# Kernel optimization log

Hardware: AMD Instinct MI355X
Metric: run time of the kernel (lower is better)

Reference implementation:

```python
import jax, jax.numpy as jnp
import numpy as np

CAPSULE_WIDE = 8
CAPSULE_TALL = 4
FEAT = 784
FV = FEAT // CAPSULE_TALL  # 196
B = 32768


def _linear_params(key, out_dim, in_dim):
    kw, kb = jax.random.split(key)
    bound = 1.0 / np.sqrt(in_dim)
    W = jax.random.uniform(kw, (out_dim, in_dim), minval=-bound, maxval=bound, dtype=jnp.float32)
    b = jax.random.uniform(kb, (out_dim,), minval=-bound, maxval=bound, dtype=jnp.float32)
    return W, b


def setup_inputs() -> dict:
    key = jax.random.key(0)
    ks = jax.random.split(key, 7)
    x = jax.random.normal(ks[0], (B, FEAT), dtype=jnp.float32)
    W1, b1 = _linear_params(ks[1], FV, FV)
    W2, b2 = _linear_params(ks[2], FV, FV)
    W3, b3 = _linear_params(ks[3], FV, FV)
    Wd1, bd1 = _linear_params(ks[4], FEAT, FEAT)
    Wd2, bd2 = _linear_params(ks[5], FEAT, FEAT)
    Wo, bo = _linear_params(ks[6], 10, FEAT)
    return {"x": x, "W1": W1, "b1": b1, "W2": W2, "b2": b2, "W3": W3, "b3": b3,
            "Wd1": Wd1, "bd1": bd1, "Wd2": Wd2, "bd2": bd2, "Wo": Wo, "bo": bo}


def reference(x, W1, b1, W2, b2, W3, b3, Wd1, bd1, Wd2, bd2, Wo, bo):
    h = x  # [B, 784]
    for _ in range(CAPSULE_WIDE):
        v = h.reshape(h.shape[0], CAPSULE_TALL, FV)  # [B, T, FV]
        q = v @ W1.T + b1  # first_copy
        k = v @ W2.T + b2  # second_copy
        u = v @ W3.T + b3  # third_copy
        scores = jnp.einsum('btf,bsf->bts', q, k)  # [B, T, T], unscaled
        probs = jax.nn.softmax(scores, axis=-1)
        h = jnp.einsum('bts,bsf->btf', probs, u).reshape(h.shape[0], -1)
    dec = jax.nn.relu(h @ Wd1.T + bd1) @ Wd2.T + bd2  # output_decoder
    return jax.nn.softmax(dec @ Wo.T + bo, axis=-1)  # output_probability
```

## Files before the change

### kernel.cpp

```cpp
#include <hip/hip_runtime.h>
#include <math.h>

#define NT 256
#define NTC 512
typedef _Float16 f16;
typedef _Float16 half8 __attribute__((ext_vector_type(8)));
typedef _Float16 half4 __attribute__((ext_vector_type(4)));
typedef float floatx4 __attribute__((ext_vector_type(4)));

#define ROWSHR_ADD(v, N) \
  (v) += __int_as_float(__builtin_amdgcn_update_dpp(0, __float_as_int(v), 0x110 | (N), 0xF, 0xF, true))

#define WD1_OFF  0
#define WD2_OFF  1433600
#define WOT_OFF  2867200
#define D8_OFF   2917376
#define HBUF_OFF 2918400
#define D1_OFF   55347200
#define WPKH_OFF 55347200
#define WPKL_OFF 56185856
#define SSE      38464

__device__ inline void glds16(const void* g, void* l) {
  __builtin_amdgcn_global_load_lds((const __attribute__((address_space(1))) void*)g,
                                   (__attribute__((address_space(3))) void*)l, 16, 0, 0);
}

__global__ void k_prep_wd(const float* __restrict__ Wd, f16* __restrict__ W16) {
  int idx = blockIdx.x * NT + threadIdx.x;
  if (idx >= 896 * 800) return;
  int n = idx / 800, k = idx - n * 800;
  W16[idx] = (f16)((n < 784 && k < 784) ? Wd[n * 784 + k] : 0.f);
}

__global__ void k_prep_wo(const float* __restrict__ Wo, float* __restrict__ WoT) {
  int idx = blockIdx.x * NT + threadIdx.x;
  if (idx >= 784 * 16) return;
  int f = idx >> 4, n = idx & 15;
  WoT[idx] = (n < 10) ? Wo[n * 784 + f] : 0.f;
}

__global__ void k_mm(const float* __restrict__ A0, const float* __restrict__ B0,
                     float* __restrict__ C0, int ta, int tb, int sA, int sB, int sC) {
  const float* A = A0 + (size_t)blockIdx.y * sA;
  const float* B = B0 + (size_t)blockIdx.y * sB;
  float*       C = C0 + (size_t)blockIdx.y * sC;
  __shared__ float red[256];
  const int tid = threadIdx.x;
  const int o = blockIdx.x * 64 + (tid & 63);
  const int ks = tid >> 6;
  float s = 0.f;
  int p = 0, r = 0;
  if (o < 196 * 196) {
    p = o / 196; r = o - p * 196;
    const int c0 = ks * 49;
    #pragma unroll 7
    for (int c = c0; c < c0 + 49; ++c) {
      float a = ta ? A[c * 196 + p] : A[p * 196 + c];
      float b = tb ? B[r * 196 + c] : B[c * 196 + r];
      s += a * b;
    }
  }
  red[tid] = s;
  __syncthreads();
  if (tid < 64 && o < 196 * 196)
    C[p * 196 + r] = red[tid] + red[tid + 64] + red[tid + 128] + red[tid + 192];
}

__global__ void k_prep_gq(const float* __restrict__ W1, const float* __restrict__ W2,
                          const float* __restrict__ W3, float* __restrict__ scr) {
  if (blockIdx.x < 601) {
    __shared__ float red[256];
    const int tid = threadIdx.x;
    const int o = blockIdx.x * 64 + (tid & 63);
    const int ks = tid >> 6;
    float s = 0.f;
    int p = 0, r = 0;
    if (o < 196 * 196) {
      p = o / 196; r = o - p * 196;
      const int c0 = ks * 49;
      #pragma unroll 7
      for (int c = c0; c < c0 + 49; ++c)
        s += W1[c * 196 + p] * W2[c * 196 + r];
    }
    red[tid] = s;
    __syncthreads();
    if (tid < 64 && o < 196 * 196)
      scr[p * 196 + r] = red[tid] + red[tid + 64] + red[tid + 128] + red[tid + 192];
  } else {
    int idx = (blockIdx.x - 601) * NT + threadIdx.x;
    if (idx < 196 * 196) scr[(size_t)SSE + idx] = W3[idx];
  }
}

__global__ void k_prep_vec(const float* __restrict__ W2, const float* __restrict__ b1,
                           const float* __restrict__ b3,
                           const float* __restrict__ G, const float* __restrict__ Qbase,
                           float* __restrict__ gtab, float* __restrict__ d8out) {
  __shared__ float z[196], cj[196], d[196], tmp[196];
  const int i = blockIdx.x;
  const int tid = threadIdx.x;
  const float* W3 = Qbase;
  for (int t = tid; t < 196; t += NT) {
    float s = 0.f;
    for (int f = 0; f < 196; ++f) s += b1[f] * W2[f * 196 + t];
    z[t] = s;
    d[t] = 0.f;
    cj[t] = b3[t];
  }
  __syncthreads();
  for (int j = 0; j < i; ++j) {
    for (int t = tid; t < 196; t += NT) {
      float s = 0.f;
      for (int c = 0; c < 196; ++c) s += W3[t * 196 + c] * cj[c];
      tmp[t] = s;
      d[t] += cj[t];
    }
    __syncthreads();
    for (int t = tid; t < 196; t += NT) cj[t] = tmp[t];
    __syncthreads();
  }
  if (i == 7) {
    for (int t = tid; t < 196; t += NT) d8out[t] = d[t] + cj[t];
  }
  for (int t = tid; t < 196; t += NT) {
    float s = z[t];
    for (int k = 0; k < 196; ++k) s += G[k * 196 + t] * d[k];
    tmp[t] = s;
  }
  __syncthreads();
  for (int t = tid; t < 196; t += NT) {
    float s;
    if (i == 0) {
      s = tmp[t];
    } else {
      const float* Qi = Qbase + (size_t)(i - 1) * SSE;
      s = 0.f;
      for (int n = 0; n < 196; ++n) s += Qi[n * 196 + t] * tmp[n];
    }
    gtab[i * 196 + t] = s;
  }
}

__global__ void k_prep_pack(const float* __restrict__ scr,
                            f16* __restrict__ Wph, f16* __restrict__ Wpl) {
  int idx = blockIdx.x * NT + threadIdx.x;
  if (idx >= 9 * 208 * 224) return;
  int s = idx / (208 * 224), rem = idx - s * (208 * 224);
  int n = rem / 224, k = rem - n * 224;
  float v = 0.f;
  if (k < 196) {
    if (n < 196) {
      if (s == 8) {
        v = scr[(size_t)8 * SSE + n * 196 + k];
      } else {
        const float* M = (s == 0) ? scr : (scr + (size_t)(16 + s - 1) * SSE);
        v = M[k * 196 + n];
      }
    } else if (n == 196 && s < 8) {
      v = scr[(size_t)23 * SSE + s * 196 + k];
    }
  }
  f16 hi = (f16)v;
  Wph[idx] = hi;
  Wpl[idx] = (f16)(v - (float)hi);
}

__global__ __launch_bounds__(NTC, 4)
void k_caps(const float* __restrict__ x,
            const f16* __restrict__ Wph, const f16* __restrict__ Wpl,
            const float* __restrict__ d8g,
            f16* __restrict__ hbuf) {
  __shared__ __align__(16) char smem[72704];
  f16*   vAhi = (f16*)smem;
  f16*   vAlo = (f16*)(smem + 29696);
  float* Sful = (float*)(smem + 59392);
  float* Rl   = (float*)(smem + 69632);
  float* Cm   = (float*)(smem + 71680);

  const int tid  = threadIdx.x;
  const int w    = tid >> 6;
  const int lane = tid & 63;
  const int l15  = lane & 15;
  const int quad = lane >> 4;
  const int e0   = blockIdx.x * 16;
  const bool haveJ1 = (w + 8) < 13;

  for (int idx = tid; idx < 16 * 196; idx += NTC) {
    int elem = idx / 196, g = idx - elem * 196;
    int t = g / 49, f = (g - t * 49) * 4;
    floatx4 v4 = *(const floatx4*)&x[(size_t)(e0 + elem) * 784 + g * 4];
    half4 h4, l4;
    #pragma unroll
    for (int q = 0; q < 4; ++q) {
      f16 h = (f16)v4[q];
      h4[q] = h;
      l4[q] = (f16)(v4[q] - (float)h);
    }
    int vo = (elem * 4 + t) * 232 + f;
    *(half4*)&vAhi[vo] = h4;
    *(half4*)&vAlo[vo] = l4;
  }
  for (int p = tid; p < 64 * 36; p += NTC) {
    int row = p / 36, c = 196 + (p - (p / 36) * 36);
    vAhi[row * 232 + c] = (f16)0;
    vAlo[row * 232 + c] = (f16)0;
  }
  for (int p = tid; p < 8 * 16 * 20; p += NTC) Sful[p] = 0.f;
  __syncthreads();

  float vv0[4][4], vv1[4][4];
  {
    int c0 = w * 16 + l15;
    int c1 = 128 + w * 16 + l15;
    #pragma unroll
    for (int mt = 0; mt < 4; ++mt)
      #pragma unroll
      for (int s = 0; s < 4; ++s) {
        int ro = ((mt * 4 + quad) * 4 + s) * 232;
        vv0[mt][s] = (float)vAhi[ro + c0] + (float)vAlo[ro + c0];
        vv1[mt][s] = haveJ1 ? ((float)vAhi[ro + c1] + (float)vAlo[ro + c1]) : 0.f;
      }
  }

  #pragma unroll 2
  for (int i = 0; i < 8; ++i) {
    floatx4 acc0[4], acc1[4];
    #pragma unroll
    for (int mt = 0; mt < 4; ++mt) {
      acc0[mt] = (floatx4){0.f, 0.f, 0.f, 0.f};
      acc1[mt] = (floatx4){0.f, 0.f, 0.f, 0.f};
    }
    const int wb0 = ((i * 208 + w * 16 + l15) * 224) + quad * 8;
    const int wb1 = ((i * 208 + (w + 8) * 16 + l15) * 224) + quad * 8;
    #pragma unroll
    for (int ks = 0; ks < 7; ++ks) {
      half8 ah[4], al[4];
      #pragma unroll
      for (int mt = 0; mt < 4; ++mt) {
        int ao = (mt * 16 + l15) * 232 + ks * 32 + quad * 8;
        ah[mt] = *(const half8*)&vAhi[ao];
        al[mt] = *(const half8*)&vAlo[ao];
      }
      {
        half8 bh = *(const half8*)&Wph[wb0 + ks * 32];
        half8 bl = *(const half8*)&Wpl[wb0 + ks * 32];
        #pragma unroll
        for (int mt = 0; mt < 4; ++mt) {
          acc0[mt] = __builtin_amdgcn_mfma_f32_16x16x32_f16(ah[mt], bh, acc0[mt], 0, 0, 0);
          acc0[mt] = __builtin_amdgcn_mfma_f32_16x16x32_f16(ah[mt], bl, acc0[mt], 0, 0, 0);
          acc0[mt] = __builtin_amdgcn_mfma_f32_16x16x32_f16(al[mt], bh, acc0[mt], 0, 0, 0);
        }
      }
      if (haveJ1) {
        half8 bh = *(const half8*)&Wph[wb1 + ks * 32];
        half8 bl = *(const half8*)&Wpl[wb1 + ks * 32];
        #pragma unroll
        for (int mt = 0; mt < 4; ++mt) {
          acc1[mt] = __builtin_amdgcn_mfma_f32_16x16x32_f16(ah[mt], bh, acc1[mt], 0, 0, 0);
          acc1[mt] = __builtin_amdgcn_mfma_f32_16x16x32_f16(ah[mt], bl, acc1[mt], 0, 0, 0);
          acc1[mt] = __builtin_amdgcn_mfma_f32_16x16x32_f16(al[mt], bh, acc1[mt], 0, 0, 0);
        }
      }
    }
    #pragma unroll
    for (int mt = 0; mt < 4; ++mt) {
      float part[16];
      #pragma unroll
      for (int t = 0; t < 4; ++t)
        #pragma unroll
        for (int s = 0; s < 4; ++s)
          part[t * 4 + s] = acc0[mt][t] * vv0[mt][s] + acc1[mt][t] * vv1[mt][s];
      #pragma unroll
      for (int p = 0; p < 16; ++p) {
        ROWSHR_ADD(part[p], 8);
        ROWSHR_ADD(part[p], 4);
        ROWSHR_ADD(part[p], 2);
        ROWSHR_ADD(part[p], 1);
      }
      if (l15 == 0) {
        int elem = mt * 4 + quad;
        #pragma unroll
        for (int t = 0; t < 4; ++t)
          #pragma unroll
          for (int s = 0; s < 4; ++s)
            atomicAdd(&Sful[(i * 16 + elem) * 20 + t * 4 + s], part[t * 4 + s]);
      }
    }
    if (w == 4 && l15 == 4) {
      #pragma unroll
      for (int mt = 0; mt < 4; ++mt)
        *(floatx4*)&Rl[i * 64 + mt * 16 + quad * 4] = acc1[mt];
    }
  }
  __syncthreads();

  if (tid < 16) {
    const int e = tid;
    float C[4][4] = {{1,0,0,0},{0,1,0,0},{0,0,1,0},{0,0,0,1}};
    #pragma unroll 1
    for (int i = 0; i < 8; ++i) {
      float M[4][4];
      #pragma unroll
      for (int a = 0; a < 4; ++a) {
        floatx4 mm = *(const floatx4*)&Sful[(i * 16 + e) * 20 + a * 4];
        #pragma unroll
        for (int b = 0; b < 4; ++b) M[a][b] = mm[b];
      }
      floatx4 rv = *(const floatx4*)&Rl[i * 64 + e * 4];
      float T1[4][4], Cr[4];
      #pragma unroll
      for (int t = 0; t < 4; ++t)
        #pragma unroll
        for (int b = 0; b < 4; ++b)
          T1[t][b] = C[t][0]*M[0][b] + C[t][1]*M[1][b] + C[t][2]*M[2][b] + C[t][3]*M[3][b];
      #pragma unroll
      for (int s = 0; s < 4; ++s)
        Cr[s] = C[s][0]*rv[0] + C[s][1]*rv[1] + C[s][2]*rv[2] + C[s][3]*rv[3];
      float P[4][4];
      #pragma unroll
      for (int t = 0; t < 4; ++t) {
        float S[4];
        #pragma unroll
        for (int s = 0; s < 4; ++s)
          S[s] = T1[t][0]*C[s][0] + T1[t][1]*C[s][1] + T1[t][2]*C[s][2] + T1[t][3]*C[s][3] + Cr[s];
        float m = fmaxf(fmaxf(S[0], S[1]), fmaxf(S[2], S[3]));
        float e0_ = __expf(S[0] - m), e1 = __expf(S[1] - m);
        float e2 = __expf(S[2] - m), e3 = __expf(S[3] - m);
        float inv = 1.f / (e0_ + e1 + e2 + e3);
        P[t][0] = e0_ * inv; P[t][1] = e1 * inv; P[t][2] = e2 * inv; P[t][3] = e3 * inv;
      }
      float Cn[4][4];
      #pragma unroll
      for (int t = 0; t < 4; ++t)
        #pragma unroll
        for (int s = 0; s < 4; ++s)
          Cn[t][s] = P[t][0]*C[0][s] + P[t][1]*C[1][s] + P[t][2]*C[2][s] + P[t][3]*C[3][s];
      #pragma unroll
      for (int t = 0; t < 4; ++t)
        #pragma unroll
        for (int s = 0; s < 4; ++s) C[t][s] = Cn[t][s];
    }
    #pragma unroll
    for (int t = 0; t < 4; ++t)
      *(floatx4*)&Cm[e * 16 + t * 4] = (floatx4){C[t][0], C[t][1], C[t][2], C[t][3]};
  }
  __syncthreads();

  {
    floatx4 acu0[4], acu1[4];
    #pragma unroll
    for (int mt = 0; mt < 4; ++mt) {
      acu0[mt] = (floatx4){0.f, 0.f, 0.f, 0.f};
      acu1[mt] = (floatx4){0.f, 0.f, 0.f, 0.f};
    }
    const int wb0 = ((8 * 208 + w * 16 + l15) * 224) + quad * 8;
    const int wb1 = ((8 * 208 + (w + 8) * 16 + l15) * 224) + quad * 8;
    #pragma unroll
    for (int ks = 0; ks < 7; ++ks) {
      half8 ah[4], al[4];
      #pragma unroll
      for (int mt = 0; mt < 4; ++mt) {
        int ao = (mt * 16 + l15) * 232 + ks * 32 + quad * 8;
        ah[mt] = *(const half8*)&vAhi[ao];
        al[mt] = *(const half8*)&vAlo[ao];
      }
      {
        half8 bh = *(const half8*)&Wph[wb0 + ks * 32];
        half8 bl = *(const half8*)&Wpl[wb0 + ks * 32];
        #pragma unroll
        for (int mt = 0; mt < 4; ++mt) {
          acu0[mt] = __builtin_amdgcn_mfma_f32_16x16x32_f16(ah[mt], bh, acu0[mt], 0, 0, 0);
          acu0[mt] = __builtin_amdgcn_mfma_f32_16x16x32_f16(ah[mt], bl, acu0[mt], 0, 0, 0);
          acu0[mt] = __builtin_amdgcn_mfma_f32_16x16x32_f16(al[mt], bh, acu0[mt], 0, 0, 0);
        }
      }
      if (haveJ1) {
        half8 bh = *(const half8*)&Wph[wb1 + ks * 32];
        half8 bl = *(const half8*)&Wpl[wb1 + ks * 32];
        #pragma unroll
        for (int mt = 0; mt < 4; ++mt) {
          acu1[mt] = __builtin_amdgcn_mfma_f32_16x16x32_f16(ah[mt], bh, acu1[mt], 0, 0, 0);
          acu1[mt] = __builtin_amdgcn_mfma_f32_16x16x32_f16(ah[mt], bl, acu1[mt], 0, 0, 0);
          acu1[mt] = __builtin_amdgcn_mfma_f32_16x16x32_f16(al[mt], bh, acu1[mt], 0, 0, 0);
        }
      }
    }
    const int f0 = w * 16 + l15;
    const int f1 = 128 + w * 16 + l15;
    const bool doF1 = haveJ1 && (f1 < 196);
    float d80 = d8g[f0];
    float d81 = doF1 ? d8g[f1] : 0.f;
    #pragma unroll
    for (int mt = 0; mt < 4; ++mt) {
      int elem = mt * 4 + quad;
      floatx4 c0 = *(const floatx4*)&Cm[elem * 16 + 0];
      floatx4 c1 = *(const floatx4*)&Cm[elem * 16 + 4];
      floatx4 c2 = *(const floatx4*)&Cm[elem * 16 + 8];
      floatx4 c3 = *(const floatx4*)&Cm[elem * 16 + 12];
      {
        floatx4 u = acu0[mt];
        float h0 = c0[0]*u[0] + c0[1]*u[1] + c0[2]*u[2] + c0[3]*u[3] + d80;
        float h1 = c1[0]*u[0] + c1[1]*u[1] + c1[2]*u[2] + c1[3]*u[3] + d80;
        float h2 = c2[0]*u[0] + c2[1]*u[1] + c2[2]*u[2] + c2[3]*u[3] + d80;
        float h3 = c3[0]*u[0] + c3[1]*u[1] + c3[2]*u[2] + c3[3]*u[3] + d80;
        size_t base = (size_t)(e0 + elem) * 800;
        hbuf[base + 0 * 196 + f0] = (f16)h0;
        hbuf[base + 1 * 196 + f0] = (f16)h1;
        hbuf[base + 2 * 196 + f0] = (f16)h2;
        hbuf[base + 3 * 196 + f0] = (f16)h3;
      }
      if (doF1) {
        floatx4 u = acu1[mt];
        float h0 = c0[0]*u[0] + c0[1]*u[1] + c0[2]*u[2] + c0[3]*u[3] + d81;
        float h1 = c1[0]*u[0] + c1[1]*u[1] + c1[2]*u[2] + c1[3]*u[3] + d81;
        float h2 = c2[0]*u[0] + c2[1]*u[1] + c2[2]*u[2] + c2[3]*u[3] + d81;
        float h3 = c3[0]*u[0] + c3[1]*u[1] + c3[2]*u[2] + c3[3]*u[3] + d81;
        size_t base = (size_t)(e0 + elem) * 800;
        hbuf[base + 0 * 196 + f1] = (f16)h0;
        hbuf[base + 1 * 196 + f1] = (f16)h1;
        hbuf[base + 2 * 196 + f1] = (f16)h2;
        hbuf[base + 3 * 196 + f1] = (f16)h3;
      }
    }
  }
  for (int idx = tid; idx < 256; idx += NTC)
    hbuf[(size_t)(e0 + (idx >> 4)) * 800 + 784 + (idx & 15)] = (f16)0;
}

__global__ __launch_bounds__(NT, 2)
void k_dec(const f16* __restrict__ A, const f16* __restrict__ Bw,
           const float* __restrict__ bias, f16* __restrict__ C, int do_relu) {
  __shared__ __align__(16) f16 As[128 * 32];
  __shared__ __align__(16) f16 Bs[128 * 32];
  const int tid = threadIdx.x, w = tid >> 6, lane = tid & 63;
  const int l15 = lane & 15, quad = lane >> 4;
  const int m0 = blockIdx.x * 128, n0 = blockIdx.y * 128;
  const int wm = w & 1, wn = w >> 1;
  const int srow = lane >> 2, soff = (lane & 3) * 8;

  floatx4 acc[4][4];
  #pragma unroll
  for (int nt = 0; nt < 4; ++nt) {
    int col = n0 + wn * 64 + nt * 16 + l15;
    float bb = (col < 784) ? bias[col] : 0.f;
    #pragma unroll
    for (int mt = 0; mt < 4; ++mt) acc[mt][nt] = (floatx4){bb, bb, bb, bb};
  }

  for (int kk = 0; kk < 25; ++kk) {
    __syncthreads();
    #pragma unroll
    for (int i = 0; i < 2; ++i) {
      int r = w * 32 + i * 16;
      glds16(&A[(size_t)(m0 + r + srow) * 800 + kk * 32 + soff], &As[r * 32]);
      glds16(&Bw[(size_t)(n0 + r + srow) * 800 + kk * 32 + soff], &Bs[r * 32]);
    }
    __syncthreads();
    half8 af[4], bf[4];
    #pragma unroll
    for (int mt = 0; mt < 4; ++mt)
      af[mt] = *(const half8*)&As[(wm * 64 + mt * 16 + l15) * 32 + quad * 8];
    #pragma unroll
    for (int nt = 0; nt < 4; ++nt)
      bf[nt] = *(const half8*)&Bs[(wn * 64 + nt * 16 + l15) * 32 + quad * 8];
    #pragma unroll
    for (int mt = 0; mt < 4; ++mt)
      #pragma unroll
      for (int nt = 0; nt < 4; ++nt)
        acc[mt][nt] = __builtin_amdgcn_mfma_f32_16x16x32_f16(af[mt], bf[nt], acc[mt][nt], 0, 0, 0);
  }

  #pragma unroll
  for (int nt = 0; nt < 4; ++nt) {
    int gcol = n0 + wn * 64 + nt * 16 + l15;
    if (gcol < 800) {
      #pragma unroll
      for (int mt = 0; mt < 4; ++mt) {
        #pragma unroll
        for (int r = 0; r < 4; ++r) {
          int grow = m0 + wm * 64 + mt * 16 + quad * 4 + r;
          float v = acc[mt][nt][r];
          if (do_relu) v = fmaxf(v, 0.f);
          C[(size_t)grow * 800 + gcol] = (f16)v;
        }
      }
    }
  }
}

__global__ __launch_bounds__(NT, 4)
void k_logits(const f16* __restrict__ d2, const float* __restrict__ WoT,
              const float* __restrict__ bo, float* __restrict__ out) {
  __shared__ __align__(16) f16 ds[16 * 800];
  __shared__ float lg[160];
  const int tid = threadIdx.x;
  const size_t e0 = (size_t)blockIdx.x * 16;
  for (int i = tid; i < 16 * 98; i += NT) {
    int e = i / 98, c = (i - e * 98) * 8;
    *(half8*)&ds[e * 800 + c] = *(const half8*)&d2[(e0 + e) * 800 + c];
  }
  __syncthreads();
  {
    int e = tid >> 4, n = tid & 15;
    const f16* dp = &ds[e * 800];
    float s = 0.f;
    #pragma unroll 4
    for (int f = 0; f < 784; ++f) s += (float)dp[f] * WoT[f * 16 + n];
    if (n < 10) lg[e * 10 + n] = s + bo[n];
  }
  __syncthreads();
  if (tid < 16) {
    float l[10], m = -1e30f;
    #pragma unroll
    for (int n = 0; n < 10; ++n) { l[n] = lg[tid * 10 + n]; m = fmaxf(m, l[n]); }
    float sum = 0.f;
    #pragma unroll
    for (int n = 0; n < 10; ++n) { l[n] = __expf(l[n] - m); sum += l[n]; }
    float inv = 1.f / sum;
    #pragma unroll
    for (int n = 0; n < 10; ++n) out[(e0 + tid) * 10 + n] = l[n] * inv;
  }
}

extern "C" void kernel_launch(void* const* d_in, const int* in_sizes, int n_in,
                              void* d_out, int out_size, void* d_ws, size_t ws_size,
                              hipStream_t stream) {
  const float* x   = (const float*)d_in[0];
  const float* W1  = (const float*)d_in[1];
  const float* b1  = (const float*)d_in[2];
  const float* W2  = (const float*)d_in[3];
  const float* W3  = (const float*)d_in[5];
  const float* b3  = (const float*)d_in[6];
  const float* Wd1 = (const float*)d_in[7];
  const float* bd1 = (const float*)d_in[8];
  const float* Wd2 = (const float*)d_in[9];
  const float* bd2 = (const float*)d_in[10];
  const float* Wo  = (const float*)d_in[11];
  const float* bo  = (const float*)d_in[12];
  float* out = (float*)d_out;

  char* ws = (char*)d_ws;
  f16*   Wd1p  = (f16*)(ws + WD1_OFF);
  f16*   Wd2p  = (f16*)(ws + WD2_OFF);
  float* WoTws = (float*)(ws + WOT_OFF);
  float* d8ws  = (float*)(ws + D8_OFF);
  f16*   hbuf  = (f16*)(ws + HBUF_OFF);
  f16*   d1buf = (f16*)(ws + D1_OFF);
  f16*   Wph   = (f16*)(ws + WPKH_OFF);
  f16*   Wpl   = (f16*)(ws + WPKL_OFF);
  float* scr   = (float*)(ws + HBUF_OFF);

  const int GSK = (196 * 196 + 63) / 64;
  const int GCP = (196 * 196 + NT - 1) / NT;

  k_prep_wd<<<(896 * 800 + NT - 1) / NT, NT, 0, stream>>>(Wd1, Wd1p);
  k_prep_wd<<<(896 * 800 + NT - 1) / NT, NT, 0, stream>>>(Wd2, Wd2p);
  k_prep_wo<<<(784 * 16 + NT - 1) / NT, NT, 0, stream>>>(Wo, WoTws);

  k_prep_gq<<<GSK + GCP, NT, 0, stream>>>(W1, W2, W3, scr);
  k_mm<<<dim3(GSK, 1), NT, 0, stream>>>(W3, W3, scr + (size_t)2 * SSE, 0, 0, 0, 0, 0);
  k_mm<<<dim3(GSK, 2), NT, 0, stream>>>(scr + (size_t)2 * SSE, scr + (size_t)1 * SSE,
                                        scr + (size_t)3 * SSE, 0, 0, 0, SSE, SSE);
  k_mm<<<dim3(GSK, 4), NT, 0, stream>>>(scr + (size_t)4 * SSE, scr + (size_t)1 * SSE,
                                        scr + (size_t)5 * SSE, 0, 0, 0, SSE, SSE);
  k_mm<<<dim3(GSK, 7), NT, 0, stream>>>(scr + (size_t)1 * SSE, scr,
                                        scr + (size_t)9 * SSE, 1, 0, SSE, 0, SSE);
  k_mm<<<dim3(GSK, 7), NT, 0, stream>>>(scr + (size_t)9 * SSE, scr + (size_t)1 * SSE,
                                        scr + (size_t)16 * SSE, 0, 0, SSE, SSE, SSE);
  k_prep_vec<<<8, NT, 0, stream>>>(W2, b1, b3, scr, scr + (size_t)1 * SSE,
                                   scr + (size_t)23 * SSE, d8ws);
  k_prep_pack<<<(9 * 208 * 224 + NT - 1) / NT, NT, 0, stream>>>(scr, Wph, Wpl);

  k_caps<<<32768 / 16, NTC, 0, stream>>>(x, Wph, Wpl, d8ws, hbuf);
  k_dec<<<dim3(32768 / 128, 7), NT, 0, stream>>>(hbuf, Wd1p, bd1, d1buf, 1);
  k_dec<<<dim3(32768 / 128, 7), NT, 0, stream>>>(d1buf, Wd2p, bd2, hbuf, 0);
  k_logits<<<32768 / 16, NT, 0, stream>>>(hbuf, WoTws, bo, out);
}
```

Before: 858.4 us.

## Batch prep kernels into fewer launches and retune caps, dec, logits kernels

```diff
diff --git a/kernel.cpp b/kernel.cpp
--- a/kernel.cpp
+++ b/kernel.cpp
@@ -14,11 +14,11 @@
 #define WD1_OFF  0
 #define WD2_OFF  1433600
 #define WOT_OFF  2867200
-#define D8_OFF   2917376
-#define HBUF_OFF 2918400
-#define D1_OFF   55347200
-#define WPKH_OFF 55347200
-#define WPKL_OFF 56185856
+#define D8_OFF   2918400
+#define HBUF_OFF 2919424
+#define D1_OFF   55348224
+#define WPKH_OFF 55348224
+#define WPKL_OFF 56186880
 #define SSE      38464
 
 __device__ inline void glds16(const void* g, void* l) {
@@ -26,120 +26,145 @@
                                    (__attribute__((address_space(3))) void*)l, 16, 0, 0);
 }
 
-__global__ void k_prep_wd(const float* __restrict__ Wd, f16* __restrict__ W16) {
-  int idx = blockIdx.x * NT + threadIdx.x;
-  if (idx >= 896 * 800) return;
-  int n = idx / 800, k = idx - n * 800;
-  W16[idx] = (f16)((n < 784 && k < 784) ? Wd[n * 784 + k] : 0.f);
-}
-
-__global__ void k_prep_wo(const float* __restrict__ Wo, float* __restrict__ WoT) {
-  int idx = blockIdx.x * NT + threadIdx.x;
-  if (idx >= 784 * 16) return;
-  int f = idx >> 4, n = idx & 15;
-  WoT[idx] = (n < 10) ? Wo[n * 784 + f] : 0.f;
-}
-
-__global__ void k_mm(const float* __restrict__ A0, const float* __restrict__ B0,
-                     float* __restrict__ C0, int ta, int tb, int sA, int sB, int sC) {
-  const float* A = A0 + (size_t)blockIdx.y * sA;
-  const float* B = B0 + (size_t)blockIdx.y * sB;
-  float*       C = C0 + (size_t)blockIdx.y * sC;
+__global__ void k_prep_io(const float* __restrict__ Wd1, const float* __restrict__ Wd2,
+                          const float* __restrict__ Wo,
+                          f16* __restrict__ W1p, f16* __restrict__ W2p,
+                          float* __restrict__ WoT) {
+  int b = blockIdx.x;
+  if (b < 5600) {
+    const float* Wd = (b < 2800) ? Wd1 : Wd2;
+    f16* W16 = (b < 2800) ? W1p : W2p;
+    int idx = (b % 2800) * NT + threadIdx.x;
+    if (idx < 896 * 800) {
+      int n = idx / 800, k = idx - n * 800;
+      W16[idx] = (f16)((n < 784 && k < 784) ? Wd[n * 784 + k] : 0.f);
+    }
+  } else {
+    int idx = (b - 5600) * NT + threadIdx.x;
+    if (idx < 16 * 800) {
+      int n = idx / 800, f = idx - n * 800;
+      WoT[idx] = (n < 10 && f < 784) ? Wo[n * 784 + f] : 0.f;
+    }
+  }
+}
+
+__global__ void k_prep_gq(const float* __restrict__ W1, const float* __restrict__ W2,
+                          const float* __restrict__ W3, float* __restrict__ scr) {
   __shared__ float red[256];
   const int tid = threadIdx.x;
-  const int o = blockIdx.x * 64 + (tid & 63);
-  const int ks = tid >> 6;
+  int b = blockIdx.x;
+  if (b < 1202) {
+    int ta = (b < 601);
+    const float* A = ta ? W1 : W3;
+    const float* B = ta ? W2 : W3;
+    float* C = ta ? scr : (scr + (size_t)2 * SSE);
+    int u = ta ? b : (b - 601);
+    int o = u * 64 + (tid & 63);
+    int ks = tid >> 6;
+    float s = 0.f;
+    int p = 0, r = 0;
+    if (o < 38416) {
+      p = o / 196; r = o - p * 196;
+      const int c0 = ks * 49;
+      #pragma unroll 7
+      for (int c = c0; c < c0 + 49; ++c) {
+        float a = ta ? A[c * 196 + p] : A[p * 196 + c];
+        s += a * B[c * 196 + r];
+      }
+    }
+    red[tid] = s;
+    __syncthreads();
+    if (tid < 64 && o < 38416)
+      C[p * 196 + r] = red[tid] + red[tid + 64] + red[tid + 128] + red[tid + 192];
+  } else {
+    int idx = (b - 1202) * NT + tid;
+    if (idx < 38416) scr[(size_t)SSE + idx] = W3[idx];
+  }
+}
+
+__constant__ int MMA[4][8] = {{2,2,1,2,0,0,0,0},{4,4,4,4,3,4,9,10},
+                              {5,6,7,11,12,0,0,0},{13,14,15,0,0,0,0,0}};
+__constant__ int MMB[4][8] = {{1,2,0,0,0,0,0,0},{1,2,3,4,0,0,1,2},
+                              {0,0,0,3,4,0,0,0},{5,6,7,0,0,0,0,0}};
+__constant__ int MMC[4][8] = {{3,4,9,10,0,0,0,0},{5,6,7,8,11,12,16,17},
+                              {13,14,15,18,19,0,0,0},{20,21,22,0,0,0,0,0}};
+__constant__ int MMT[4][8] = {{0,0,1,1,0,0,0,0},{0,0,0,0,1,1,0,0},
+                              {1,1,1,0,0,0,0,0},{0,0,0,0,0,0,0,0}};
+
+__global__ __launch_bounds__(NT, 4)
+void k_mmb(float* __restrict__ scr, int stage,
+           const float* __restrict__ W2, const float* __restrict__ b1,
+           const float* __restrict__ b3, float* __restrict__ d8out) {
+  __shared__ float red[256];
+  __shared__ float z[196], cj[196], dd[196], tmp[196];
+  const int tid = threadIdx.x;
+  const int y = blockIdx.y;
+
+  if (stage == 2 && y == 5) {
+    if (blockIdx.x >= 8) return;
+    const int i = blockIdx.x;
+    const float* G = scr;
+    const float* Qbase = scr + (size_t)SSE;
+    float* gtab = scr + (size_t)23 * SSE;
+    const float* W3c = Qbase;
+    for (int t = tid; t < 196; t += NT) {
+      float s = 0.f;
+      for (int f = 0; f < 196; ++f) s += b1[f] * W2[f * 196 + t];
+      z[t] = s; dd[t] = 0.f; cj[t] = b3[t];
+    }
+    __syncthreads();
+    for (int j = 0; j < i; ++j) {
+      for (int t = tid; t < 196; t += NT) {
+        float s = 0.f;
+        for (int c = 0; c < 196; ++c) s += W3c[t * 196 + c] * cj[c];
+        tmp[t] = s; dd[t] += cj[t];
+      }
+      __syncthreads();
+      for (int t = tid; t < 196; t += NT) cj[t] = tmp[t];
+      __syncthreads();
+    }
+    if (i == 7)
+      for (int t = tid; t < 196; t += NT) d8out[t] = dd[t] + cj[t];
+    for (int t = tid; t < 196; t += NT) {
+      float s = z[t];
+      for (int k = 0; k < 196; ++k) s += G[k * 196 + t] * dd[k];
+      tmp[t] = s;
+    }
+    __syncthreads();
+    for (int t = tid; t < 196; t += NT) {
+      float s;
+      if (i == 0) s = tmp[t];
+      else {
+        const float* Qi = Qbase + (size_t)(i - 1) * SSE;
+        s = 0.f;
+        for (int n = 0; n < 196; ++n) s += Qi[n * 196 + t] * tmp[n];
+      }
+      gtab[i * 196 + t] = s;
+    }
+    return;
+  }
+
+  const float* A = scr + (size_t)MMA[stage][y] * SSE;
+  const float* B = scr + (size_t)MMB[stage][y] * SSE;
+  float*       C = scr + (size_t)MMC[stage][y] * SSE;
+  const int ta = MMT[stage][y];
+  int o = blockIdx.x * 64 + (tid & 63);
+  int ks = tid >> 6;
   float s = 0.f;
   int p = 0, r = 0;
-  if (o < 196 * 196) {
+  if (o < 38416) {
     p = o / 196; r = o - p * 196;
     const int c0 = ks * 49;
     #pragma unroll 7
     for (int c = c0; c < c0 + 49; ++c) {
       float a = ta ? A[c * 196 + p] : A[p * 196 + c];
-      float b = tb ? B[r * 196 + c] : B[c * 196 + r];
-      s += a * b;
+      s += a * B[c * 196 + r];
     }
   }
   red[tid] = s;
   __syncthreads();
-  if (tid < 64 && o < 196 * 196)
+  if (tid < 64 && o < 38416)
     C[p * 196 + r] = red[tid] + red[tid + 64] + red[tid + 128] + red[tid + 192];
-}
-
-__global__ void k_prep_gq(const float* __restrict__ W1, const float* __restrict__ W2,
-                          const float* __restrict__ W3, float* __restrict__ scr) {
-  if (blockIdx.x < 601) {
-    __shared__ float red[256];
-    const int tid = threadIdx.x;
-    const int o = blockIdx.x * 64 + (tid & 63);
-    const int ks = tid >> 6;
-    float s = 0.f;
-    int p = 0, r = 0;
-    if (o < 196 * 196) {
-      p = o / 196; r = o - p * 196;
-      const int c0 = ks * 49;
-      #pragma unroll 7
-      for (int c = c0; c < c0 + 49; ++c)
-        s += W1[c * 196 + p] * W2[c * 196 + r];
-    }
-    red[tid] = s;
-    __syncthreads();
-    if (tid < 64 && o < 196 * 196)
-      scr[p * 196 + r] = red[tid] + red[tid + 64] + red[tid + 128] + red[tid + 192];
-  } else {
-    int idx = (blockIdx.x - 601) * NT + threadIdx.x;
-    if (idx < 196 * 196) scr[(size_t)SSE + idx] = W3[idx];
-  }
-}
-
-__global__ void k_prep_vec(const float* __restrict__ W2, const float* __restrict__ b1,
-                           const float* __restrict__ b3,
-                           const float* __restrict__ G, const float* __restrict__ Qbase,
-                           float* __restrict__ gtab, float* __restrict__ d8out) {
-  __shared__ float z[196], cj[196], d[196], tmp[196];
-  const int i = blockIdx.x;
-  const int tid = threadIdx.x;
-  const float* W3 = Qbase;
-  for (int t = tid; t < 196; t += NT) {
-    float s = 0.f;
-    for (int f = 0; f < 196; ++f) s += b1[f] * W2[f * 196 + t];
-    z[t] = s;
-    d[t] = 0.f;
-    cj[t] = b3[t];
-  }
-  __syncthreads();
-  for (int j = 0; j < i; ++j) {
-    for (int t = tid; t < 196; t += NT) {
-      float s = 0.f;
-      for (int c = 0; c < 196; ++c) s += W3[t * 196 + c] * cj[c];
-      tmp[t] = s;
-      d[t] += cj[t];
-    }
-    __syncthreads();
-    for (int t = tid; t < 196; t += NT) cj[t] = tmp[t];
-    __syncthreads();
-  }
-  if (i == 7) {
-    for (int t = tid; t < 196; t += NT) d8out[t] = d[t] + cj[t];
-  }
-  for (int t = tid; t < 196; t += NT) {
-    float s = z[t];
-    for (int k = 0; k < 196; ++k) s += G[k * 196 + t] * d[k];
-    tmp[t] = s;
-  }
-  __syncthreads();
-  for (int t = tid; t < 196; t += NT) {
-    float s;
-    if (i == 0) {
-      s = tmp[t];
-    } else {
-      const float* Qi = Qbase + (size_t)(i - 1) * SSE;
-      s = 0.f;
-      for (int n = 0; n < 196; ++n) s += Qi[n * 196 + t] * tmp[n];
-    }
-    gtab[i * 196 + t] = s;
-  }
 }
 
 __global__ void k_prep_pack(const float* __restrict__ scr,
@@ -151,9 +176,8 @@
   float v = 0.f;
   if (k < 196) {
     if (n < 196) {
-      if (s == 8) {
-        v = scr[(size_t)8 * SSE + n * 196 + k];
-      } else {
+      if (s == 8) v = scr[(size_t)8 * SSE + n * 196 + k];
+      else {
         const float* M = (s == 0) ? scr : (scr + (size_t)(16 + s - 1) * SSE);
         v = M[k * 196 + n];
       }
@@ -171,12 +195,12 @@
             const f16* __restrict__ Wph, const f16* __restrict__ Wpl,
             const float* __restrict__ d8g,
             f16* __restrict__ hbuf) {
-  __shared__ __align__(16) char smem[72704];
+  __shared__ __align__(16) char smem[70656];
   f16*   vAhi = (f16*)smem;
   f16*   vAlo = (f16*)(smem + 29696);
   float* Sful = (float*)(smem + 59392);
-  float* Rl   = (float*)(smem + 69632);
-  float* Cm   = (float*)(smem + 71680);
+  float* Rl   = (float*)(smem + 67584);
+  float* Cm   = (float*)(smem + 69632);
 
   const int tid  = threadIdx.x;
   const int w    = tid >> 6;
@@ -206,7 +230,7 @@
     vAhi[row * 232 + c] = (f16)0;
     vAlo[row * 232 + c] = (f16)0;
   }
-  for (int p = tid; p < 8 * 16 * 20; p += NTC) Sful[p] = 0.f;
+  for (int p = tid; p < 2048; p += NTC) Sful[p] = 0.f;
   __syncthreads();
 
   float vv0[4][4], vv1[4][4];
@@ -223,7 +247,7 @@
       }
   }
 
-  #pragma unroll 2
+  #pragma unroll 1
   for (int i = 0; i < 8; ++i) {
     floatx4 acc0[4], acc1[4];
     #pragma unroll
@@ -284,7 +308,7 @@
         for (int t = 0; t < 4; ++t)
           #pragma unroll
           for (int s = 0; s < 4; ++s)
-            atomicAdd(&Sful[(i * 16 + elem) * 20 + t * 4 + s], part[t * 4 + s]);
+            atomicAdd(&Sful[((i * 16 + elem) * 4 + t) * 4 + s], part[t * 4 + s]);
       }
     }
     if (w == 4 && l15 == 4) {
@@ -303,7 +327,7 @@
       float M[4][4];
       #pragma unroll
       for (int a = 0; a < 4; ++a) {
-        floatx4 mm = *(const floatx4*)&Sful[(i * 16 + e) * 20 + a * 4];
+        floatx4 mm = *(const floatx4*)&Sful[((i * 16 + e) * 4 + a) * 4];
         #pragma unroll
         for (int b = 0; b < 4; ++b) M[a][b] = mm[b];
       }
@@ -428,7 +452,7 @@
     hbuf[(size_t)(e0 + (idx >> 4)) * 800 + 784 + (idx & 15)] = (f16)0;
 }
 
-__global__ __launch_bounds__(NT, 2)
+__global__ __launch_bounds__(NT, 4)
 void k_dec(const f16* __restrict__ A, const f16* __restrict__ Bw,
            const float* __restrict__ bias, f16* __restrict__ C, int do_relu) {
   __shared__ __align__(16) f16 As[128 * 32];
@@ -504,9 +528,16 @@
   {
     int e = tid >> 4, n = tid & 15;
     const f16* dp = &ds[e * 800];
+    const float* wt = &WoT[n * 800];
     float s = 0.f;
-    #pragma unroll 4
-    for (int f = 0; f < 784; ++f) s += (float)dp[f] * WoT[f * 16 + n];
+    #pragma unroll 2
+    for (int f = 0; f < 784; f += 8) {
+      half8 d8 = *(const half8*)&dp[f];
+      floatx4 wa = *(const floatx4*)&wt[f];
+      floatx4 wb = *(const floatx4*)&wt[f + 4];
+      s += (float)d8[0]*wa[0] + (float)d8[1]*wa[1] + (float)d8[2]*wa[2] + (float)d8[3]*wa[3]
+         + (float)d8[4]*wb[0] + (float)d8[5]*wb[1] + (float)d8[6]*wb[2] + (float)d8[7]*wb[3];
+    }
     if (n < 10) lg[e * 10 + n] = s + bo[n];
   }
   __syncthreads();
@@ -551,25 +582,12 @@
   f16*   Wpl   = (f16*)(ws + WPKL_OFF);
   float* scr   = (float*)(ws + HBUF_OFF);
 
-  const int GSK = (196 * 196 + 63) / 64;
-  const int GCP = (196 * 196 + NT - 1) / NT;
-
-  k_prep_wd<<<(896 * 800 + NT - 1) / NT, NT, 0, stream>>>(Wd1, Wd1p);
-  k_prep_wd<<<(896 * 800 + NT - 1) / NT, NT, 0, stream>>>(Wd2, Wd2p);
-  k_prep_wo<<<(784 * 16 + NT - 1) / NT, NT, 0, stream>>>(Wo, WoTws);
-
-  k_prep_gq<<<GSK + GCP, NT, 0, stream>>>(W1, W2, W3, scr);
-  k_mm<<<dim3(GSK, 1), NT, 0, stream>>>(W3, W3, scr + (size_t)2 * SSE, 0, 0, 0, 0, 0);
-  k_mm<<<dim3(GSK, 2), NT, 0, stream>>>(scr + (size_t)2 * SSE, scr + (size_t)1 * SSE,
-                                        scr + (size_t)3 * SSE, 0, 0, 0, SSE, SSE);
-  k_mm<<<dim3(GSK, 4), NT, 0, stream>>>(scr + (size_t)4 * SSE, scr + (size_t)1 * SSE,
-                                        scr + (size_t)5 * SSE, 0, 0, 0, SSE, SSE);
-  k_mm<<<dim3(GSK, 7), NT, 0, stream>>>(scr + (size_t)1 * SSE, scr,
-                                        scr + (size_t)9 * SSE, 1, 0, SSE, 0, SSE);
-  k_mm<<<dim3(GSK, 7), NT, 0, stream>>>(scr + (size_t)9 * SSE, scr + (size_t)1 * SSE,
-                                        scr + (size_t)16 * SSE, 0, 0, SSE, SSE, SSE);
-  k_prep_vec<<<8, NT, 0, stream>>>(W2, b1, b3, scr, scr + (size_t)1 * SSE,
-                                   scr + (size_t)23 * SSE, d8ws);
+  k_prep_io<<<5650, NT, 0, stream>>>(Wd1, Wd2, Wo, Wd1p, Wd2p, WoTws);
+  k_prep_gq<<<1353, NT, 0, stream>>>(W1, W2, W3, scr);
+  k_mmb<<<dim3(601, 4), NT, 0, stream>>>(scr, 0, W2, b1, b3, d8ws);
+  k_mmb<<<dim3(601, 8), NT, 0, stream>>>(scr, 1, W2, b1, b3, d8ws);
+  k_mmb<<<dim3(601, 6), NT, 0, stream>>>(scr, 2, W2, b1, b3, d8ws);
+  k_mmb<<<dim3(601, 3), NT, 0, stream>>>(scr, 3, W2, b1, b3, d8ws);
   k_prep_pack<<<(9 * 208 * 224 + NT - 1) / NT, NT, 0, stream>>>(scr, Wph, Wpl);
 
   k_caps<<<32768 / 16, NTC, 0, stream>>>(x, Wph, Wpl, d8ws, hbuf);
```

Measured after the change: 1.028 ms. +19.8%, slower.
